# Kernel tuning notes

Hardware: AMD Instinct MI355X
Metric: run time of the kernel (lower is better)

Reference implementation:

```python
import jax, jax.numpy as jnp
import numpy as np

HIDDEN = 128
N_NODES = 200000
N_VISITED = 1024


def setup_inputs() -> dict:
    key = jax.random.key(0)
    ks = jax.random.split(key, 7)
    X = jax.random.normal(ks[0], (N_NODES, HIDDEN), dtype=jnp.float32)
    x = jax.random.normal(ks[1], (HIDDEN,), dtype=jnp.float32)
    s = 1.0 / np.sqrt(HIDDEN)
    Wq = jax.random.uniform(ks[2], (3 * HIDDEN, HIDDEN), jnp.float32, -s, s)
    Wk = jax.random.uniform(ks[3], (HIDDEN, HIDDEN), jnp.float32, -s, s)
    Wv = jax.random.uniform(ks[4], (HIDDEN, HIDDEN), jnp.float32, -s, s)
    Wo = jax.random.uniform(ks[5], (HIDDEN, HIDDEN), jnp.float32, -s, s)
    nodes_visited = jax.random.randint(ks[6], (N_VISITED,), 0, N_NODES, dtype=jnp.int32)
    return {
        "X": X, "x": x, "Wq": Wq, "Wk": Wk, "Wv": Wv, "Wo": Wo,
        "nodes_visited": nodes_visited,
        "starting_node": 0, "previous_node": 1,
    }


def reference(X, x, Wq, Wk, Wv, Wo, nodes_visited, starting_node, previous_node):
    # X: [n_nodes, 128]; x: [128]
    n_nodes = X.shape[0]
    # features_concat = [x ; X[start] ; X[prev]]  -> [3*128]
    features_concat = jnp.concatenate([x, X[starting_node], X[previous_node]])
    q = features_concat @ Wq              # [128]
    k = X @ Wk                            # [n_nodes, 128]
    v = X @ Wv                            # [n_nodes, 128]
    u = (k @ q) / jnp.sqrt(jnp.float32(HIDDEN))   # [n_nodes]
    # additive mask: 1 everywhere, 0 at visited nodes (faithful to original)
    mask = jnp.ones((n_nodes,), dtype=X.dtype).at[nodes_visited].set(0.0)
    # final_layer == False branch
    u_ = jax.nn.softmax(u + mask)         # [n_nodes]
    h = u_ @ v                            # [128]
    out = h @ Wo                          # [128]
    return out
```

## Files before the change

### kernel.cpp

```cpp
#include <hip/hip_runtime.h>
#include <math.h>

#define HIDDEN 128
#define MAIN_BLOCKS 512
#define MAIN_THREADS 1024
#define MAX_BMAP_WORDS 6272

__global__ __launch_bounds__(512) void prep_kernel(
    const float* __restrict__ X, const float* __restrict__ x,
    const float* __restrict__ Wq, const float* __restrict__ Wk,
    const int* __restrict__ startp, const int* __restrict__ prevp,
    float* __restrict__ qk)
{
    __shared__ float fc[384];
    __shared__ float qpart[4][HIDDEN];
    __shared__ float qv[HIDDEN];
    const int t   = threadIdx.x;
    const int col = t & (HIDDEN - 1);
    const int seg = t >> 7;

    if (t < 128)       fc[t]       = x[t];
    else if (t < 256)  fc[t]       = X[(size_t)startp[0] * HIDDEN + (t - 128)];
    else if (t < 384)  fc[t]       = X[(size_t)prevp[0]  * HIDDEN + (t - 256)];
    __syncthreads();

    float acc = 0.f;
    const int m0 = seg * 96;
    #pragma unroll 8
    for (int m = 0; m < 96; ++m)
        acc += fc[m0 + m] * Wq[(size_t)(m0 + m) * HIDDEN + col];
    qpart[seg][col] = acc;
    __syncthreads();
    if (t < HIDDEN)
        qv[t] = qpart[0][t] + qpart[1][t] + qpart[2][t] + qpart[3][t];
    __syncthreads();

    const int hw  = t >> 5;
    const int sub = t & 31;
    const float4 qv4 = *(const float4*)(&qv[sub << 2]);
    for (int row = hw; row < HIDDEN; row += 16) {
        const float4 wk4 = *(const float4*)(Wk + (size_t)row * HIDDEN + (sub << 2));
        float p = wk4.x * qv4.x + wk4.y * qv4.y + wk4.z * qv4.z + wk4.w * qv4.w;
        #pragma unroll
        for (int off = 16; off >= 1; off >>= 1)
            p += __shfl_xor(p, off, 64);
        if (sub == 0) qk[row] = p * 0.08838834764831845f;
    }
}

__global__ __launch_bounds__(MAIN_THREADS) void main_kernel(
    const float* __restrict__ X, const int* __restrict__ visited, int nv,
    const float* __restrict__ qk,
    float* __restrict__ Mb, float* __restrict__ Sb, float* __restrict__ Gb,
    int n)
{
    __shared__ unsigned bmap[MAX_BMAP_WORDS];
    __shared__ float m_arr[32];
    __shared__ float s_arr[32];
    __shared__ float g_all[32 * HIDDEN];

    const int tid  = threadIdx.x;
    const int lane = tid & 63;
    const int sub  = lane & 31;
    const int half = (lane >> 5) & 1;
    const int wavesPerBlock = blockDim.x >> 6;
    const int gw  = blockIdx.x * wavesPerBlock + (tid >> 6);
    const int vhw = gw * 2 + half;
    const int T   = gridDim.x * wavesPerBlock * 2;

    const int nwords = (n + 31) >> 5;
    for (int w = tid; w < nwords; w += blockDim.x) bmap[w] = 0u;
    __syncthreads();
    for (int i = tid; i < nv; i += blockDim.x) {
        const int v = visited[i];
        atomicOr(&bmap[v >> 5], 1u << (v & 31));
    }
    __syncthreads();

    const float4 qkv = *(const float4*)(qk + (sub << 2));

    float m = -INFINITY, s = 0.f;
    float g0 = 0.f, g1 = 0.f, g2 = 0.f, g3 = 0.f;

    for (int r = vhw; r < n; r += T) {
        const float4 xv = *(const float4*)(X + (size_t)r * HIDDEN + (sub << 2));
        float p = xv.x * qkv.x + xv.y * qkv.y + xv.z * qkv.z + xv.w * qkv.w;
        #pragma unroll
        for (int off = 16; off >= 1; off >>= 1)
            p += __shfl_xor(p, off, 64);
        const float maskv = ((bmap[r >> 5] >> (r & 31)) & 1u) ? 0.f : 1.f;
        const float u = p + maskv;
        const float mn    = fmaxf(m, u);
        const float scale = __expf(m - mn);
        const float w     = __expf(u - mn);
        s  = s  * scale + w;
        g0 = g0 * scale + w * xv.x;
        g1 = g1 * scale + w * xv.y;
        g2 = g2 * scale + w * xv.z;
        g3 = g3 * scale + w * xv.w;
        m  = mn;
    }

    const int hw = tid >> 5;
    *(float4*)(&g_all[hw * HIDDEN + (sub << 2)]) = make_float4(g0, g1, g2, g3);
    if (sub == 0) { m_arr[hw] = m; s_arr[hw] = s; }
    __syncthreads();

    float mb = m_arr[0];
    #pragma unroll
    for (int h = 1; h < 32; ++h) mb = fmaxf(mb, m_arr[h]);

    if (tid < HIDDEN) {
        float G = 0.f;
        #pragma unroll 4
        for (int h = 0; h < 32; ++h)
            G += g_all[h * HIDDEN + tid] * __expf(m_arr[h] - mb);
        Gb[blockIdx.x * HIDDEN + tid] = G;
    } else if (tid == HIDDEN) {
        float S = 0.f;
        #pragma unroll
        for (int h = 0; h < 32; ++h) S += s_arr[h] * __expf(m_arr[h] - mb);
        Sb[blockIdx.x] = S;
        Mb[blockIdx.x] = mb;
    }
}

__global__ __launch_bounds__(512) void finish_kernel(
    const float* __restrict__ Mb, const float* __restrict__ Sb,
    const float* __restrict__ Gb,
    const float* __restrict__ Wv, const float* __restrict__ Wo,
    float* __restrict__ out, int B)
{
    __shared__ float red[512];
    __shared__ float e[MAIN_BLOCKS];
    __shared__ float part[4][HIDDEN];
    __shared__ float pvec[HIDDEN];
    __shared__ float hvec[HIDDEN];
    const int t   = threadIdx.x;
    const int col = t & (HIDDEN - 1);
    const int seg = t >> 7;

    const float mt = (t < B) ? Mb[t] : -INFINITY;
    red[t] = mt; __syncthreads();
    for (int st = 256; st >= 1; st >>= 1) {
        if (t < st) red[t] = fmaxf(red[t], red[t + st]);
        __syncthreads();
    }
    const float M = red[0];
    __syncthreads();

    float ls = 0.f;
    if (t < B) { const float eb = __expf(mt - M); e[t] = eb; ls = Sb[t] * eb; }
    red[t] = ls; __syncthreads();
    for (int st = 256; st >= 1; st >>= 1) {
        if (t < st) red[t] += red[t + st];
        __syncthreads();
    }
    const float S = red[0];
    __syncthreads();

    {
        float acc = 0.f;
        const int b0 = seg * (B >> 2);
        #pragma unroll 8
        for (int b = 0; b < (MAIN_BLOCKS >> 2); ++b)
            acc += Gb[(size_t)(b0 + b) * HIDDEN + col] * e[b0 + b];
        part[seg][col] = acc;
    }
    __syncthreads();
    if (t < HIDDEN)
        pvec[t] = (part[0][t] + part[1][t] + part[2][t] + part[3][t]) / S;
    __syncthreads();

    {
        float acc = 0.f;
        const int m0 = seg * 32;
        #pragma unroll 8
        for (int m = 0; m < 32; ++m)
            acc += pvec[m0 + m] * Wv[(size_t)(m0 + m) * HIDDEN + col];
        part[seg][col] = acc;
    }
    __syncthreads();
    if (t < HIDDEN)
        hvec[t] = part[0][t] + part[1][t] + part[2][t] + part[3][t];
    __syncthreads();

    {
        float acc = 0.f;
        const int m0 = seg * 32;
        #pragma unroll 8
        for (int m = 0; m < 32; ++m)
            acc += hvec[m0 + m] * Wo[(size_t)(m0 + m) * HIDDEN + col];
        part[seg][col] = acc;
    }
    __syncthreads();
    if (t < HIDDEN)
        out[t] = part[0][t] + part[1][t] + part[2][t] + part[3][t];
}

extern "C" void kernel_launch(void* const* d_in, const int* in_sizes, int n_in,
                              void* d_out, int out_size, void* d_ws, size_t ws_size,
                              hipStream_t stream)
{
    const float* X       = (const float*)d_in[0];
    const float* x       = (const float*)d_in[1];
    const float* Wq      = (const float*)d_in[2];
    const float* Wk      = (const float*)d_in[3];
    const float* Wv      = (const float*)d_in[4];
    const float* Wo      = (const float*)d_in[5];
    const int*   visited = (const int*)d_in[6];
    const int*   startp  = (const int*)d_in[7];
    const int*   prevp   = (const int*)d_in[8];

    const int n  = in_sizes[0] / HIDDEN;
    const int nv = in_sizes[6];

    float* ws = (float*)d_ws;
    float* qk = ws;
    float* Mb = ws + 128;
    float* Sb = Mb + MAIN_BLOCKS;
    float* Gb = Sb + MAIN_BLOCKS;

    prep_kernel<<<1, 512, 0, stream>>>(X, x, Wq, Wk, startp, prevp, qk);
    main_kernel<<<MAIN_BLOCKS, MAIN_THREADS, 0, stream>>>(X, visited, nv, qk, Mb, Sb, Gb, n);
    finish_kernel<<<1, 512, 0, stream>>>(Mb, Sb, Gb, Wv, Wo, (float*)d_out, MAIN_BLOCKS);
}
```

Measured before the change: 187.4 us.

## Fuse prep, main and finish kernels into one with last-block reduction

The three launches are merged into a single kernel. Every block recomputes the query projection (q and Wk·q) redundantly in shared memory, overlapping this with building the visited bitmap. An atomic counter elects the last finishing block to do the cross-block softmax merge and the Wv/Wo projections. This removes two kernel launches and the serial gaps between them, but adds a memset, redundant per-block Wq/Wk reads, and a threadfence/atomic tail.

```diff
diff --git a/kernel.cpp b/kernel.cpp
--- a/kernel.cpp
+++ b/kernel.cpp
@@ -2,82 +2,85 @@
 #include <math.h>
 
 #define HIDDEN 128
-#define MAIN_BLOCKS 512
-#define MAIN_THREADS 1024
-#define MAX_BMAP_WORDS 6272
-
-__global__ __launch_bounds__(512) void prep_kernel(
+#define NBLOCKS 512
+#define NTHREADS 1024
+#define BMAP_WORDS 6272
+
+__global__ __launch_bounds__(NTHREADS, 8) void fused_kernel(
     const float* __restrict__ X, const float* __restrict__ x,
     const float* __restrict__ Wq, const float* __restrict__ Wk,
+    const float* __restrict__ Wv, const float* __restrict__ Wo,
+    const int* __restrict__ visited, int nv,
     const int* __restrict__ startp, const int* __restrict__ prevp,
-    float* __restrict__ qk)
+    float* __restrict__ Mb, float* __restrict__ Sb, float* __restrict__ Gb,
+    unsigned* __restrict__ counter,
+    float* __restrict__ out, int n)
 {
+    __shared__ unsigned bmap[BMAP_WORDS];
     __shared__ float fc[384];
-    __shared__ float qpart[4][HIDDEN];
+    __shared__ float qpart[8][HIDDEN];
     __shared__ float qv[HIDDEN];
-    const int t   = threadIdx.x;
-    const int col = t & (HIDDEN - 1);
-    const int seg = t >> 7;
-
-    if (t < 128)       fc[t]       = x[t];
-    else if (t < 256)  fc[t]       = X[(size_t)startp[0] * HIDDEN + (t - 128)];
-    else if (t < 384)  fc[t]       = X[(size_t)prevp[0]  * HIDDEN + (t - 256)];
-    __syncthreads();
-
-    float acc = 0.f;
-    const int m0 = seg * 96;
-    #pragma unroll 8
-    for (int m = 0; m < 96; ++m)
-        acc += fc[m0 + m] * Wq[(size_t)(m0 + m) * HIDDEN + col];
-    qpart[seg][col] = acc;
-    __syncthreads();
-    if (t < HIDDEN)
-        qv[t] = qpart[0][t] + qpart[1][t] + qpart[2][t] + qpart[3][t];
-    __syncthreads();
-
-    const int hw  = t >> 5;
-    const int sub = t & 31;
-    const float4 qv4 = *(const float4*)(&qv[sub << 2]);
-    for (int row = hw; row < HIDDEN; row += 16) {
-        const float4 wk4 = *(const float4*)(Wk + (size_t)row * HIDDEN + (sub << 2));
-        float p = wk4.x * qv4.x + wk4.y * qv4.y + wk4.z * qv4.z + wk4.w * qv4.w;
-        #pragma unroll
-        for (int off = 16; off >= 1; off >>= 1)
-            p += __shfl_xor(p, off, 64);
-        if (sub == 0) qk[row] = p * 0.08838834764831845f;
-    }
-}
-
-__global__ __launch_bounds__(MAIN_THREADS) void main_kernel(
-    const float* __restrict__ X, const int* __restrict__ visited, int nv,
-    const float* __restrict__ qk,
-    float* __restrict__ Mb, float* __restrict__ Sb, float* __restrict__ Gb,
-    int n)
-{
-    __shared__ unsigned bmap[MAX_BMAP_WORDS];
-    __shared__ float m_arr[32];
-    __shared__ float s_arr[32];
+    __shared__ float qk_s[HIDDEN];
+    __shared__ float m_arr[32], s_arr[32];
     __shared__ float g_all[32 * HIDDEN];
+    __shared__ bool  is_last;
 
     const int tid  = threadIdx.x;
     const int lane = tid & 63;
     const int sub  = lane & 31;
     const int half = (lane >> 5) & 1;
-    const int wavesPerBlock = blockDim.x >> 6;
+    const int col  = tid & (HIDDEN - 1);
+    const int seg  = tid >> 7;
+
+    const int nwords = (n + 31) >> 5;
+    for (int w = tid; w < nwords; w += NTHREADS) bmap[w] = 0u;
+    if (tid < 128)       fc[tid] = x[tid];
+    else if (tid < 256)  fc[tid] = X[(size_t)startp[0] * HIDDEN + (tid - 128)];
+    else if (tid < 384)  fc[tid] = X[(size_t)prevp[0]  * HIDDEN + (tid - 256)];
+    __syncthreads();
+
+    for (int i = tid; i < nv; i += NTHREADS) {
+        const int v = visited[i];
+        atomicOr(&bmap[v >> 5], 1u << (v & 31));
+    }
+
+    {
+        float acc = 0.f;
+        const int m0 = seg * 48;
+        #pragma unroll 8
+        for (int m = 0; m < 48; ++m)
+            acc += fc[m0 + m] * Wq[(size_t)(m0 + m) * HIDDEN + col];
+        qpart[seg][col] = acc;
+    }
+    __syncthreads();
+    if (tid < HIDDEN) {
+        float s = 0.f;
+        #pragma unroll
+        for (int k = 0; k < 8; ++k) s += qpart[k][tid];
+        qv[tid] = s;
+    }
+    __syncthreads();
+
+    {
+        const int hw32 = tid >> 5;
+        const float4 qv4 = *(const float4*)(&qv[sub << 2]);
+        for (int row = hw32; row < HIDDEN; row += 32) {
+            const float4 wk4 = *(const float4*)(Wk + (size_t)row * HIDDEN + (sub << 2));
+            float p = wk4.x * qv4.x + wk4.y * qv4.y + wk4.z * qv4.z + wk4.w * qv4.w;
+            #pragma unroll
+            for (int off = 16; off >= 1; off >>= 1)
+                p += __shfl_xor(p, off, 64);
+            if (sub == 0) qk_s[row] = p * 0.08838834764831845f;
+        }
+    }
+    __syncthreads();
+
+    const int wavesPerBlock = NTHREADS >> 6;
     const int gw  = blockIdx.x * wavesPerBlock + (tid >> 6);
     const int vhw = gw * 2 + half;
-    const int T   = gridDim.x * wavesPerBlock * 2;
-
-    const int nwords = (n + 31) >> 5;
-    for (int w = tid; w < nwords; w += blockDim.x) bmap[w] = 0u;
-    __syncthreads();
-    for (int i = tid; i < nv; i += blockDim.x) {
-        const int v = visited[i];
-        atomicOr(&bmap[v >> 5], 1u << (v & 31));
-    }
-    __syncthreads();
-
-    const float4 qkv = *(const float4*)(qk + (sub << 2));
+    const int T   = NBLOCKS * wavesPerBlock * 2;
+
+    const float4 qkv = *(const float4*)(&qk_s[sub << 2]);
 
     float m = -INFINITY, s = 0.f;
     float g0 = 0.f, g1 = 0.f, g2 = 0.f, g3 = 0.f;
@@ -115,7 +118,7 @@
         #pragma unroll 4
         for (int h = 0; h < 32; ++h)
             G += g_all[h * HIDDEN + tid] * __expf(m_arr[h] - mb);
-        Gb[blockIdx.x * HIDDEN + tid] = G;
+        Gb[(size_t)blockIdx.x * HIDDEN + tid] = G;
     } else if (tid == HIDDEN) {
         float S = 0.f;
         #pragma unroll
@@ -123,37 +126,38 @@
         Sb[blockIdx.x] = S;
         Mb[blockIdx.x] = mb;
     }
-}
-
-__global__ __launch_bounds__(512) void finish_kernel(
-    const float* __restrict__ Mb, const float* __restrict__ Sb,
-    const float* __restrict__ Gb,
-    const float* __restrict__ Wv, const float* __restrict__ Wo,
-    float* __restrict__ out, int B)
-{
-    __shared__ float red[512];
-    __shared__ float e[MAIN_BLOCKS];
-    __shared__ float part[4][HIDDEN];
-    __shared__ float pvec[HIDDEN];
-    __shared__ float hvec[HIDDEN];
-    const int t   = threadIdx.x;
-    const int col = t & (HIDDEN - 1);
-    const int seg = t >> 7;
-
-    const float mt = (t < B) ? Mb[t] : -INFINITY;
-    red[t] = mt; __syncthreads();
-    for (int st = 256; st >= 1; st >>= 1) {
-        if (t < st) red[t] = fmaxf(red[t], red[t + st]);
+
+    __threadfence();
+    __syncthreads();
+    if (tid == 0) {
+        const unsigned prev = atomicAdd(counter, 1u);
+        is_last = (prev == (unsigned)(NBLOCKS - 1));
+    }
+    __syncthreads();
+    if (!is_last) return;
+    __threadfence();
+
+    float* e   = g_all;
+    float* red = g_all + NBLOCKS;
+
+    const float mt = (tid < NBLOCKS) ? Mb[tid] : -INFINITY;
+    if (tid < NBLOCKS) red[tid] = mt;
+    __syncthreads();
+    for (int st = NBLOCKS / 2; st >= 1; st >>= 1) {
+        if (tid < st) red[tid] = fmaxf(red[tid], red[tid + st]);
         __syncthreads();
     }
     const float M = red[0];
     __syncthreads();
 
-    float ls = 0.f;
-    if (t < B) { const float eb = __expf(mt - M); e[t] = eb; ls = Sb[t] * eb; }
-    red[t] = ls; __syncthreads();
-    for (int st = 256; st >= 1; st >>= 1) {
-        if (t < st) red[t] += red[t + st];
+    if (tid < NBLOCKS) {
+        const float eb = __expf(mt - M);
+        e[tid]   = eb;
+        red[tid] = Sb[tid] * eb;
+    }
+    __syncthreads();
+    for (int st = NBLOCKS / 2; st >= 1; st >>= 1) {
+        if (tid < st) red[tid] += red[tid + st];
         __syncthreads();
     }
     const float S = red[0];
@@ -161,41 +165,53 @@
 
     {
         float acc = 0.f;
-        const int b0 = seg * (B >> 2);
+        const int b0 = seg * (NBLOCKS / 8);
         #pragma unroll 8
-        for (int b = 0; b < (MAIN_BLOCKS >> 2); ++b)
+        for (int b = 0; b < NBLOCKS / 8; ++b)
             acc += Gb[(size_t)(b0 + b) * HIDDEN + col] * e[b0 + b];
-        part[seg][col] = acc;
-    }
-    __syncthreads();
-    if (t < HIDDEN)
-        pvec[t] = (part[0][t] + part[1][t] + part[2][t] + part[3][t]) / S;
-    __syncthreads();
-
-    {
-        float acc = 0.f;
-        const int m0 = seg * 32;
-        #pragma unroll 8
-        for (int m = 0; m < 32; ++m)
-            acc += pvec[m0 + m] * Wv[(size_t)(m0 + m) * HIDDEN + col];
-        part[seg][col] = acc;
-    }
-    __syncthreads();
-    if (t < HIDDEN)
-        hvec[t] = part[0][t] + part[1][t] + part[2][t] + part[3][t];
-    __syncthreads();
-
-    {
-        float acc = 0.f;
-        const int m0 = seg * 32;
-        #pragma unroll 8
-        for (int m = 0; m < 32; ++m)
-            acc += hvec[m0 + m] * Wo[(size_t)(m0 + m) * HIDDEN + col];
-        part[seg][col] = acc;
-    }
-    __syncthreads();
-    if (t < HIDDEN)
-        out[t] = part[0][t] + part[1][t] + part[2][t] + part[3][t];
+        qpart[seg][col] = acc;
+    }
+    __syncthreads();
+    if (tid < HIDDEN) {
+        float G = 0.f;
+        #pragma unroll
+        for (int k = 0; k < 8; ++k) G += qpart[k][tid];
+        qv[tid] = G / S;
+    }
+    __syncthreads();
+
+    {
+        float acc = 0.f;
+        const int m0 = seg * 16;
+        #pragma unroll
+        for (int mm = 0; mm < 16; ++mm)
+            acc += qv[m0 + mm] * Wv[(size_t)(m0 + mm) * HIDDEN + col];
+        qpart[seg][col] = acc;
+    }
+    __syncthreads();
+    if (tid < HIDDEN) {
+        float h = 0.f;
+        #pragma unroll
+        for (int k = 0; k < 8; ++k) h += qpart[k][tid];
+        qk_s[tid] = h;
+    }
+    __syncthreads();
+
+    {
+        float acc = 0.f;
+        const int m0 = seg * 16;
+        #pragma unroll
+        for (int mm = 0; mm < 16; ++mm)
+            acc += qk_s[m0 + mm] * Wo[(size_t)(m0 + mm) * HIDDEN + col];
+        qpart[seg][col] = acc;
+    }
+    __syncthreads();
+    if (tid < HIDDEN) {
+        float o = 0.f;
+        #pragma unroll
+        for (int k = 0; k < 8; ++k) o += qpart[k][tid];
+        out[tid] = o;
+    }
 }
 
 extern "C" void kernel_launch(void* const* d_in, const int* in_sizes, int n_in,
@@ -216,12 +232,13 @@
     const int nv = in_sizes[6];
 
     float* ws = (float*)d_ws;
-    float* qk = ws;
-    float* Mb = ws + 128;
-    float* Sb = Mb + MAIN_BLOCKS;
-    float* Gb = Sb + MAIN_BLOCKS;
-
-    prep_kernel<<<1, 512, 0, stream>>>(X, x, Wq, Wk, startp, prevp, qk);
-    main_kernel<<<MAIN_BLOCKS, MAIN_THREADS, 0, stream>>>(X, visited, nv, qk, Mb, Sb, Gb, n);
-    finish_kernel<<<1, 512, 0, stream>>>(Mb, Sb, Gb, Wv, Wo, (float*)d_out, MAIN_BLOCKS);
+    float* Mb = ws;
+    float* Sb = Mb + NBLOCKS;
+    float* Gb = Sb + NBLOCKS;
+    unsigned* counter = (unsigned*)(Gb + (size_t)NBLOCKS * HIDDEN);
+
+    hipMemsetAsync(counter, 0, sizeof(unsigned), stream);
+    fused_kernel<<<NBLOCKS, NTHREADS, 0, stream>>>(
+        X, x, Wq, Wk, Wv, Wo, visited, nv, startp, prevp,
+        Mb, Sb, Gb, counter, (float*)d_out, n);
 }
```

After: 353.0 us. +88.4%, slower.
